# Kernel optimization log

Measured on AMD Instinct MI355X. Metric: run time of the kernel, lower is better.

## Reference

```python
import jax, jax.numpy as jnp
import numpy as np

DIM = 1024
HEADS = 16
HEAD_DIM = DIM // HEADS
B, N = 2, 2048


def setup_inputs() -> dict:
    key = jax.random.key(0)
    k1, k2, k3, k4 = jax.random.split(key, 4)
    scale = 1.0 / np.sqrt(DIM)
    return {
        "x": jax.random.normal(k1, (B, N, DIM), dtype=jnp.float32),
        "w_qkv": jax.random.normal(k2, (DIM, 3 * DIM), dtype=jnp.float32) * scale,
        "w_out": jax.random.normal(k3, (DIM, DIM), dtype=jnp.float32) * scale,
        "b_out": jax.random.normal(k4, (DIM,), dtype=jnp.float32) * 0.01,
    }


def reference(x, w_qkv, w_out, b_out):
    b, n, c = x.shape
    h, d = HEADS, c // HEADS
    sm_scale = d ** -0.5
    qkv = x @ w_qkv  # [b, n, 3c]
    q, k, v = jnp.split(qkv, 3, axis=-1)
    # [b, n, c] -> [b, h, n, d]
    q = q.reshape(b, n, h, d).transpose(0, 2, 1, 3)
    k = k.reshape(b, n, h, d).transpose(0, 2, 1, 3)
    v = v.reshape(b, n, h, d).transpose(0, 2, 1, 3)
    dots = jnp.einsum("bhqd,bhkd->bhqk", q, k) * sm_scale
    attn = jax.nn.softmax(dots, axis=-1)
    out = jnp.einsum("bhqk,bhkd->bhqd", attn, v)
    out = out.transpose(0, 2, 1, 3).reshape(b, n, c)
    return out @ w_out + b_out
```

## Files before the change

kernel.cpp:

```cpp
#include <hip/hip_runtime.h>
#include <hip/hip_bf16.h>

typedef __attribute__((ext_vector_type(8))) short bf16x8;
typedef __attribute__((ext_vector_type(4))) float f32x4;

#define B_    2
#define N_    2048
#define DIM_  1024
#define H_    16
#define D_    64
#define BH_   32
#define QSC   0.18033688f

static __device__ __forceinline__ void gload_lds16(const void* g, void* l) {
  __builtin_amdgcn_global_load_lds((const __attribute__((address_space(1))) void*)g,
                                   (__attribute__((address_space(3))) void*)l, 16, 0, 0);
}

__global__ __launch_bounds__(256) void prep_kernel(const float* __restrict__ x,
                                                   const float* __restrict__ w_qkv,
                                                   const float* __restrict__ w_out,
                                                   __hip_bfloat16* __restrict__ xb,
                                                   __hip_bfloat16* __restrict__ wqkT,
                                                   __hip_bfloat16* __restrict__ woT) {
  __shared__ float tile[64][65];
  const int bid = blockIdx.x, t = threadIdx.x;
  if (bid < 4096) {
    const int i = bid * 256 + t;
    float4 v = reinterpret_cast<const float4*>(x)[i];
    union { __hip_bfloat16 h[4]; uint2 u; } cv;
    cv.h[0] = __float2bfloat16(v.x);
    cv.h[1] = __float2bfloat16(v.y);
    cv.h[2] = __float2bfloat16(v.z);
    cv.h[3] = __float2bfloat16(v.w);
    reinterpret_cast<uint2*>(xb)[i] = cv.u;
    return;
  }
  const float* in;
  __hip_bfloat16* out;
  int R, C, c0, r0;
  if (bid < 4096 + 768) {
    const int bx = bid - 4096;
    in = w_qkv; out = wqkT; R = 1024; C = 3072;
    c0 = (bx % 48) * 64; r0 = (bx / 48) * 64;
  } else {
    const int bx = bid - 4096 - 768;
    in = w_out; out = woT; R = 1024; C = 1024;
    c0 = (bx % 16) * 64; r0 = (bx / 16) * 64;
  }
#pragma unroll
  for (int i = 0; i < 16; ++i) {
    int idx = i * 256 + t;
    int r = idx >> 6, c = idx & 63;
    tile[r][c] = in[(size_t)(r0 + r) * C + (c0 + c)];
  }
  __syncthreads();
#pragma unroll
  for (int i = 0; i < 16; ++i) {
    int idx = i * 256 + t;
    int rr = idx >> 6, cc = idx & 63;
    out[(size_t)(c0 + rr) * R + (r0 + cc)] = __float2bfloat16(tile[cc][rr]);
  }
}

#define GEMM_CORE(A_, Bt_)                                                               \
  constexpr int K = 1024;                                                                \
  __shared__ __align__(16) __hip_bfloat16 As[128 * 64];                                  \
  __shared__ __align__(16) __hip_bfloat16 Bs[128 * 64];                                  \
  const int t = threadIdx.x, w = t >> 6, lane = t & 63;                                  \
  const int l16 = lane & 15, kg = lane >> 4;                                             \
  const int m0 = blockIdx.y * 128, n0 = blockIdx.x * 128;                                \
  const int wm = w >> 1, wn = w & 1;                                                     \
  f32x4 acc[4][4];                                                                       \
  _Pragma("unroll") for (int i = 0; i < 4; ++i)                                          \
    _Pragma("unroll") for (int j = 0; j < 4; ++j) acc[i][j] = {0.f, 0.f, 0.f, 0.f};      \
  size_t srcA[4], srcB[4];                                                               \
  _Pragma("unroll") for (int i = 0; i < 4; ++i) {                                        \
    const int c = 256 * i + t;                                                           \
    const int row = c >> 3, jsw = (c & 7) ^ (row & 7);                                   \
    srcA[i] = (size_t)(m0 + row) * K + jsw * 8;                                          \
    srcB[i] = (size_t)(n0 + row) * K + jsw * 8;                                          \
  }                                                                                      \
  for (int k0 = 0; k0 < K; k0 += 64) {                                                   \
    __syncthreads();                                                                     \
    _Pragma("unroll") for (int i = 0; i < 4; ++i) {                                      \
      gload_lds16(A_ + srcA[i] + k0, (char*)As + 4096 * i + 1024 * w);                   \
      gload_lds16(Bt_ + srcB[i] + k0, (char*)Bs + 4096 * i + 1024 * w);                  \
    }                                                                                    \
    __syncthreads();                                                                     \
    _Pragma("unroll") for (int kk = 0; kk < 2; ++kk) {                                   \
      bf16x8 a[4], b[4];                                                                 \
      _Pragma("unroll") for (int i = 0; i < 4; ++i) {                                    \
        const int row = wm * 64 + i * 16 + l16;                                          \
        const int jsw = ((kk << 2) | kg) ^ (row & 7);                                    \
        a[i] = *reinterpret_cast<const bf16x8*>((const char*)As + row * 128 + jsw * 16); \
      }                                                                                  \
      _Pragma("unroll") for (int j = 0; j < 4; ++j) {                                    \
        const int row = wn * 64 + j * 16 + l16;                                          \
        const int jsw = ((kk << 2) | kg) ^ (row & 7);                                    \
        b[j] = *reinterpret_cast<const bf16x8*>((const char*)Bs + row * 128 + jsw * 16); \
      }                                                                                  \
      _Pragma("unroll") for (int i = 0; i < 4; ++i)                                      \
        _Pragma("unroll") for (int j = 0; j < 4; ++j)                                    \
          acc[i][j] = __builtin_amdgcn_mfma_f32_16x16x32_bf16(a[i], b[j], acc[i][j], 0, 0, 0); \
    }                                                                                    \
  }

__global__ __launch_bounds__(512, 2) void gemm_qkv_kernel(const __hip_bfloat16* __restrict__ A,
                                                          const __hip_bfloat16* __restrict__ Bt,
                                                          __hip_bfloat16* __restrict__ Qw,
                                                          __hip_bfloat16* __restrict__ Kw,
                                                          __hip_bfloat16* __restrict__ Vt) {
  __shared__ __align__(16) char lds[131072];
  const int t = threadIdx.x, w = t >> 6, lane = t & 63;
  const int l16 = lane & 15, kg = lane >> 4;
  int flat = blockIdx.y * 12 + blockIdx.x;
  flat = (flat & 7) * 24 + (flat >> 3);
  const int bx = flat % 12, by = flat / 12;
  const int m0 = by * 256, n0 = bx * 256;
  const int wm = w >> 2, wn = w & 3;
  const int rA = t >> 3;
  const int jb = (t & 7) ^ (rA & 7);

#define LDSOFF(bb, mat) (((bb) * 2 + (mat)) * 32768)
#define STG_A(bb, tt, h)                                                                    \
  do {                                                                                      \
    gload_lds16(A + (size_t)(m0 + rA + 64 * (h)) * 1024 + (tt) * 64 + jb * 8,               \
                (char*)lds + LDSOFF(bb, 0) + (h) * 8192 + t * 16);                          \
    gload_lds16(A + (size_t)(m0 + rA + 64 * (h) + 128) * 1024 + (tt) * 64 + jb * 8,         \
                (char*)lds + LDSOFF(bb, 0) + (h) * 8192 + 16384 + t * 16);                  \
  } while (0)
#define STG_B(bb, tt, h)                                                                    \
  do {                                                                                      \
    gload_lds16(Bt + (size_t)(n0 + rA + 128 * (h)) * 1024 + (tt) * 64 + jb * 8,             \
                (char*)lds + LDSOFF(bb, 1) + (h) * 16384 + t * 16);                         \
    gload_lds16(Bt + (size_t)(n0 + rA + 128 * (h) + 64) * 1024 + (tt) * 64 + jb * 8,        \
                (char*)lds + LDSOFF(bb, 1) + (h) * 16384 + 8192 + t * 16);                  \
  } while (0)
#define RD_A(dst, q, i, kk)                                                                 \
  {                                                                                         \
    const int row = wm * 128 + ((q) * 2 + (i)) * 16 + l16;                                  \
    dst = *reinterpret_cast<const bf16x8*>(Ab + row * 128 + ((((kk) * 4 + kg) ^ (row & 7)) * 16)); \
  }
#define RD_B(dst, nj, kk)                                                                   \
  {                                                                                         \
    const int row = wn * 64 + (nj) * 16 + l16;                                              \
    dst = *reinterpret_cast<const bf16x8*>(Bb + row * 128 + ((((kk) * 4 + kg) ^ (row & 7)) * 16)); \
  }
#define PHASE(q)                                                                            \
  do {                                                                                      \
    bf16x8 af[2][2];                                                                        \
    _Pragma("unroll") for (int i = 0; i < 2; ++i)                                           \
      _Pragma("unroll") for (int kk = 0; kk < 2; ++kk) RD_A(af[i][kk], q, i, kk);           \
    __builtin_amdgcn_s_setprio(1);                                                          \
    _Pragma("unroll") for (int i = 0; i < 2; ++i)                                           \
      _Pragma("unroll") for (int nj = 0; nj < 4; ++nj)                                      \
        _Pragma("unroll") for (int kk = 0; kk < 2; ++kk)                                    \
          acc[(q) * 2 + i][nj] =                                                            \
              __builtin_amdgcn_mfma_f32_16x16x32_bf16(af[i][kk], bfr[nj][kk],               \
                                                      acc[(q) * 2 + i][nj], 0, 0, 0);       \
    __builtin_amdgcn_s_setprio(0);                                                          \
  } while (0)

  f32x4 acc[8][4];
#pragma unroll
  for (int i = 0; i < 8; ++i)
#pragma unroll
    for (int j = 0; j < 4; ++j) acc[i][j] = {0.f, 0.f, 0.f, 0.f};

  STG_A(0, 0, 0); STG_A(0, 0, 1); STG_B(0, 0, 0); STG_B(0, 0, 1);
  STG_B(1, 1, 0); STG_B(1, 1, 1); STG_A(1, 1, 0);

#pragma unroll 1
  for (int kt = 0; kt < 16; ++kt) {
    const int b = kt & 1;
    const char* Ab = (const char*)lds + LDSOFF(b, 0);
    const char* Bb = (const char*)lds + LDSOFF(b, 1);

    if (kt < 15) STG_A(b ^ 1, kt + 1, 1);
    __builtin_amdgcn_sched_barrier(0);
    if (kt < 15) asm volatile("s_waitcnt vmcnt(8)" ::: "memory");
    else         asm volatile("s_waitcnt vmcnt(0)" ::: "memory");
    __builtin_amdgcn_s_barrier();
    __builtin_amdgcn_sched_barrier(0);
    bf16x8 bfr[4][2];
#pragma unroll
    for (int nj = 0; nj < 4; ++nj)
#pragma unroll
      for (int kk = 0; kk < 2; ++kk) RD_B(bfr[nj][kk], nj, kk);
    PHASE(0);
    __builtin_amdgcn_s_barrier();
    __builtin_amdgcn_sched_barrier(0);

    if (kt < 14) STG_B(b, kt + 2, 0);
    __builtin_amdgcn_sched_barrier(0);
    PHASE(1);
    __builtin_amdgcn_s_barrier();
    __builtin_amdgcn_sched_barrier(0);

    if (kt < 14) STG_B(b, kt + 2, 1);
    PHASE(2);

    if (kt < 14) STG_A(b, kt + 2, 0);
    __builtin_amdgcn_sched_barrier(0);
    PHASE(3);
    __builtin_amdgcn_s_barrier();
    __builtin_amdgcn_sched_barrier(0);
  }

  const int which = n0 >> 10;
#pragma unroll
  for (int nj = 0; nj < 4; ++nj) {
    const int n = n0 + wn * 64 + nj * 16 + l16;
    const int nn = n & 1023;
    const int h = nn >> 6, d = nn & 63;
#pragma unroll
    for (int mi = 0; mi < 8; ++mi) {
      const int m = m0 + wm * 128 + mi * 16 + kg * 4;
      const int bb = m >> 11, tt = m & 2047;
      if (which == 2) {
        union { __hip_bfloat16 hh[4]; unsigned long long u; } pv;
#pragma unroll
        for (int r = 0; r < 4; ++r) pv.hh[r] = __float2bfloat16(acc[mi][nj][r]);
        *reinterpret_cast<unsigned long long*>(
            &Vt[((size_t)(bb * H_ + h) * D_ + d) * N_ + tt]) = pv.u;
      } else {
        __hip_bfloat16* dst = (which == 0) ? Qw : Kw;
        const float sc = (which == 0) ? QSC : 1.0f;
#pragma unroll
        for (int r = 0; r < 4; ++r)
          dst[((size_t)(bb * H_ + h) * N_ + tt + r) * D_ + d] = __float2bfloat16(acc[mi][nj][r] * sc);
      }
    }
  }
#undef PHASE
#undef RD_B
#undef RD_A
#undef STG_B
#undef STG_A
#undef LDSOFF
}

__global__ __launch_bounds__(256) void gemm_out_kernel(const __hip_bfloat16* __restrict__ A,
                                                       const __hip_bfloat16* __restrict__ Bt,
                                                       const float* __restrict__ bo,
                                                       float* __restrict__ out) {
  GEMM_CORE(A, Bt)

#pragma unroll
  for (int j = 0; j < 4; ++j) {
    const int n = n0 + wn * 64 + j * 16 + l16;
    const float bias = bo[n];
#pragma unroll
    for (int i = 0; i < 4; ++i) {
#pragma unroll
      for (int r = 0; r < 4; ++r) {
        const int m = m0 + wm * 64 + i * 16 + kg * 4 + r;
        out[(size_t)m * 1024 + n] = acc[i][j][r] + bias;
      }
    }
  }
}

__global__ __launch_bounds__(512) void attn_kernel(const __hip_bfloat16* __restrict__ Q,
                                                   const __hip_bfloat16* __restrict__ K,
                                                   const __hip_bfloat16* __restrict__ Vt,
                                                   __hip_bfloat16* __restrict__ O) {
  __shared__ __align__(16) __hip_bfloat16 Ks[2][64 * 64];
  __shared__ __align__(16) __hip_bfloat16 Vs[2][64 * 64];
  __shared__ __align__(16) __hip_bfloat16 Plds[8][16][64];
  const int bh = blockIdx.y;
  const int q0 = blockIdx.x * 128;
  const int t = threadIdx.x, w = t >> 6, lane = t & 63;
  const int l16 = lane & 15, kg = lane >> 4;
  const int b = bh >> 4, h = bh & 15;

  const __hip_bfloat16* Kbh = K + (size_t)bh * N_ * D_;
  const __hip_bfloat16* Vbh = Vt + (size_t)bh * D_ * N_;

  const int crow = t >> 3, cb = t & 7;
  const int csw = cb ^ (crow & 7);
  const size_t offK = (size_t)crow * D_ + csw * 8;
  const size_t offV = (size_t)crow * N_ + csw * 8;

  const __hip_bfloat16* Qp = Q + ((size_t)bh * N_ + q0 + w * 16 + l16) * D_ + kg * 8;
  const bf16x8 qf0 = *reinterpret_cast<const bf16x8*>(Qp);
  const bf16x8 qf1 = *reinterpret_cast<const bf16x8*>(Qp + 32);

  bf16x8 ones;
#pragma unroll
  for (int i = 0; i < 8; ++i) ones[i] = (short)0x3F80;

  f32x4 oaccS = {0.f, 0.f, 0.f, 0.f};
  f32x4 oacc[4];
#pragma unroll
  for (int dn = 0; dn < 4; ++dn) oacc[dn] = {0.f, 0.f, 0.f, 0.f};

#define STAGE(bufi, kv)                                                          \
  do {                                                                           \
    gload_lds16(Kbh + (size_t)(kv) * D_ + offK, (char*)Ks[bufi] + w * 1024);     \
    gload_lds16(Vbh + (kv) + offV,              (char*)Vs[bufi] + w * 1024);     \
  } while (0)

  STAGE(0, 0);
  asm volatile("s_waitcnt vmcnt(0)" ::: "memory");
  __builtin_amdgcn_s_barrier();

#pragma unroll 1
  for (int it = 0; it < N_ / 64; ++it) {
    const int buf = it & 1;
    if (it + 1 < N_ / 64) STAGE(buf ^ 1, (it + 1) * 64);

    const char* Kb = (const char*)Ks[buf];
    const char* Vb = (const char*)Vs[buf];

    f32x4 s[4];
#pragma unroll
    for (int kt = 0; kt < 4; ++kt) s[kt] = {0.f, 0.f, 0.f, 0.f};
    __builtin_amdgcn_s_setprio(1);
#pragma unroll
    for (int kt = 0; kt < 4; ++kt) {
      const int row = kt * 16 + l16;
      const int rsw = (row & 7) << 4;
      const bf16x8 k0 = *reinterpret_cast<const bf16x8*>(Kb + row * 128 + ((kg << 4) ^ rsw));
      const bf16x8 k1 = *reinterpret_cast<const bf16x8*>(Kb + row * 128 + (((4 + kg) << 4) ^ rsw));
      s[kt] = __builtin_amdgcn_mfma_f32_16x16x32_bf16(k0, qf0, s[kt], 0, 0, 0);
      s[kt] = __builtin_amdgcn_mfma_f32_16x16x32_bf16(k1, qf1, s[kt], 0, 0, 0);
    }
    __builtin_amdgcn_s_setprio(0);

    const int xm3 = (l16 & 7) << 3;
#pragma unroll
    for (int kt = 0; kt < 4; ++kt) {
      union { __hip_bfloat16 hh[4]; unsigned long long u; } pk;
#pragma unroll
      for (int r = 0; r < 4; ++r) pk.hh[r] = __float2bfloat16(__builtin_amdgcn_exp2f(s[kt][r]));
      *reinterpret_cast<unsigned long long*>(&Plds[w][l16][(16 * kt + 4 * kg) ^ xm3]) = pk.u;
    }

    __builtin_amdgcn_s_setprio(1);
#pragma unroll
    for (int kk = 0; kk < 2; ++kk) {
      const bf16x8 pa = *reinterpret_cast<const bf16x8*>(
          &Plds[w][l16][(kk * 32 + kg * 8) ^ xm3]);
      oaccS = __builtin_amdgcn_mfma_f32_16x16x32_bf16(pa, ones, oaccS, 0, 0, 0);
#pragma unroll
      for (int dn = 0; dn < 4; ++dn) {
        const int vrow = dn * 16 + l16;
        const int vsw = (vrow & 7) << 4;
        const bf16x8 vf = *reinterpret_cast<const bf16x8*>(
            Vb + vrow * 128 + ((kk * 64 + kg * 16) ^ vsw));
        oacc[dn] = __builtin_amdgcn_mfma_f32_16x16x32_bf16(pa, vf, oacc[dn], 0, 0, 0);
      }
    }
    __builtin_amdgcn_s_setprio(0);

    asm volatile("s_waitcnt vmcnt(0)" ::: "memory");
    __builtin_amdgcn_s_barrier();
  }
#undef STAGE

  float inv[4];
#pragma unroll
  for (int r = 0; r < 4; ++r) inv[r] = 1.0f / oaccS[r];
  __hip_bfloat16* Ob = O + ((size_t)b * N_ + q0 + w * 16) * DIM_ + h * D_;
#pragma unroll
  for (int dn = 0; dn < 4; ++dn)
#pragma unroll
    for (int r = 0; r < 4; ++r)
      Ob[(size_t)(kg * 4 + r) * DIM_ + dn * 16 + l16] = __float2bfloat16(oacc[dn][r] * inv[r]);
}

extern "C" void kernel_launch(void* const* d_in, const int* in_sizes, int n_in,
                              void* d_out, int out_size, void* d_ws, size_t ws_size,
                              hipStream_t stream) {
  const float* x = (const float*)d_in[0];
  const float* w_qkv = (const float*)d_in[1];
  const float* w_out = (const float*)d_in[2];
  const float* b_out = (const float*)d_in[3];
  float* out = (float*)d_out;

  __hip_bfloat16* ws = (__hip_bfloat16*)d_ws;
  __hip_bfloat16* xb = ws;
  __hip_bfloat16* wqkT = xb + (size_t)4096 * 1024;
  __hip_bfloat16* woT = wqkT + (size_t)3072 * 1024;
  __hip_bfloat16* Qw = woT + (size_t)1024 * 1024;
  __hip_bfloat16* Kw = Qw + (size_t)BH_ * N_ * D_;
  __hip_bfloat16* Vt = Kw + (size_t)BH_ * N_ * D_;
  __hip_bfloat16* Ow = Vt + (size_t)BH_ * N_ * D_;

  prep_kernel<<<5120, 256, 0, stream>>>(x, w_qkv, w_out, xb, wqkT, woT);
  gemm_qkv_kernel<<<dim3(12, 16), 512, 0, stream>>>(xb, wqkT, Qw, Kw, Vt);
  attn_kernel<<<dim3(16, 32), 512, 0, stream>>>(Qw, Kw, Vt, Ow);
  gemm_out_kernel<<<dim3(8, 32), 256, 0, stream>>>(Ow, woT, b_out, out);
}
```

Baseline: 115.3 us.

## Double-buffer out-proj GEMM, triple-buffer attention KV, and compute softmax denominators with shuffles

Replaces the single-buffered out-projection GEMM macro with a double-buffered LDS pipeline. It issues the next K-tile load before waiting on the current one and raises MFMA priority. The attention kernel moves from two to three KV buffers with a prefetch distance of two and one barrier per iteration. The row-sum MFMA against a ones vector is replaced by fp32 sums of the exp values reduced with lane shuffles at the end. This gives more load/compute overlap and fewer MFMAs, at the cost of more LDS per block (which may lower occupancy) and a denominator computed in fp32 rather than from bf16-rounded probabilities.

```diff
diff --git a/kernel.cpp b/kernel.cpp
--- a/kernel.cpp
+++ b/kernel.cpp
@@ -62,49 +62,6 @@
     out[(size_t)(c0 + rr) * R + (r0 + cc)] = __float2bfloat16(tile[cc][rr]);
   }
 }
-
-#define GEMM_CORE(A_, Bt_)                                                               \
-  constexpr int K = 1024;                                                                \
-  __shared__ __align__(16) __hip_bfloat16 As[128 * 64];                                  \
-  __shared__ __align__(16) __hip_bfloat16 Bs[128 * 64];                                  \
-  const int t = threadIdx.x, w = t >> 6, lane = t & 63;                                  \
-  const int l16 = lane & 15, kg = lane >> 4;                                             \
-  const int m0 = blockIdx.y * 128, n0 = blockIdx.x * 128;                                \
-  const int wm = w >> 1, wn = w & 1;                                                     \
-  f32x4 acc[4][4];                                                                       \
-  _Pragma("unroll") for (int i = 0; i < 4; ++i)                                          \
-    _Pragma("unroll") for (int j = 0; j < 4; ++j) acc[i][j] = {0.f, 0.f, 0.f, 0.f};      \
-  size_t srcA[4], srcB[4];                                                               \
-  _Pragma("unroll") for (int i = 0; i < 4; ++i) {                                        \
-    const int c = 256 * i + t;                                                           \
-    const int row = c >> 3, jsw = (c & 7) ^ (row & 7);                                   \
-    srcA[i] = (size_t)(m0 + row) * K + jsw * 8;                                          \
-    srcB[i] = (size_t)(n0 + row) * K + jsw * 8;                                          \
-  }                                                                                      \
-  for (int k0 = 0; k0 < K; k0 += 64) {                                                   \
-    __syncthreads();                                                                     \
-    _Pragma("unroll") for (int i = 0; i < 4; ++i) {                                      \
-      gload_lds16(A_ + srcA[i] + k0, (char*)As + 4096 * i + 1024 * w);                   \
-      gload_lds16(Bt_ + srcB[i] + k0, (char*)Bs + 4096 * i + 1024 * w);                  \
-    }                                                                                    \
-    __syncthreads();                                                                     \
-    _Pragma("unroll") for (int kk = 0; kk < 2; ++kk) {                                   \
-      bf16x8 a[4], b[4];                                                                 \
-      _Pragma("unroll") for (int i = 0; i < 4; ++i) {                                    \
-        const int row = wm * 64 + i * 16 + l16;                                          \
-        const int jsw = ((kk << 2) | kg) ^ (row & 7);                                    \
-        a[i] = *reinterpret_cast<const bf16x8*>((const char*)As + row * 128 + jsw * 16); \
-      }                                                                                  \
-      _Pragma("unroll") for (int j = 0; j < 4; ++j) {                                    \
-        const int row = wn * 64 + j * 16 + l16;                                          \
-        const int jsw = ((kk << 2) | kg) ^ (row & 7);                                    \
-        b[j] = *reinterpret_cast<const bf16x8*>((const char*)Bs + row * 128 + jsw * 16); \
-      }                                                                                  \
-      _Pragma("unroll") for (int i = 0; i < 4; ++i)                                      \
-        _Pragma("unroll") for (int j = 0; j < 4; ++j)                                    \
-          acc[i][j] = __builtin_amdgcn_mfma_f32_16x16x32_bf16(a[i], b[j], acc[i][j], 0, 0, 0); \
-    }                                                                                    \
-  }
 
 __global__ __launch_bounds__(512, 2) void gemm_qkv_kernel(const __hip_bfloat16* __restrict__ A,
                                                           const __hip_bfloat16* __restrict__ Bt,
@@ -245,7 +202,74 @@
                                                        const __hip_bfloat16* __restrict__ Bt,
                                                        const float* __restrict__ bo,
                                                        float* __restrict__ out) {
-  GEMM_CORE(A, Bt)
+  __shared__ __align__(16) char lds[65536];
+  const int t = threadIdx.x, w = t >> 6, lane = t & 63;
+  const int l16 = lane & 15, kg = lane >> 4;
+  const int m0 = blockIdx.y * 128, n0 = blockIdx.x * 128;
+  const int wm = w >> 1, wn = w & 1;
+
+  f32x4 acc[4][4];
+#pragma unroll
+  for (int i = 0; i < 4; ++i)
+#pragma unroll
+    for (int j = 0; j < 4; ++j) acc[i][j] = {0.f, 0.f, 0.f, 0.f};
+
+  size_t srcA[4], srcB[4];
+#pragma unroll
+  for (int i = 0; i < 4; ++i) {
+    const int c = 256 * i + t;
+    const int row = c >> 3, jsw = (c & 7) ^ (row & 7);
+    srcA[i] = (size_t)(m0 + row) * 1024 + jsw * 8;
+    srcB[i] = (size_t)(n0 + row) * 1024 + jsw * 8;
+  }
+#define OSTG(bb, k0)                                                          \
+  do {                                                                        \
+    _Pragma("unroll") for (int i = 0; i < 4; ++i) {                           \
+      gload_lds16(A + srcA[i] + (k0), (char*)lds + (bb) * 32768 + i * 4096 + w * 1024);          \
+      gload_lds16(Bt + srcB[i] + (k0), (char*)lds + (bb) * 32768 + 16384 + i * 4096 + w * 1024); \
+    }                                                                         \
+  } while (0)
+
+  OSTG(0, 0);
+
+#pragma unroll 1
+  for (int kt = 0; kt < 16; ++kt) {
+    const int b = kt & 1;
+    __builtin_amdgcn_s_barrier();
+    __builtin_amdgcn_sched_barrier(0);
+    if (kt + 1 < 16) OSTG(b ^ 1, (kt + 1) * 64);
+    __builtin_amdgcn_sched_barrier(0);
+    if (kt + 1 < 16) asm volatile("s_waitcnt vmcnt(8)" ::: "memory");
+    else             asm volatile("s_waitcnt vmcnt(0)" ::: "memory");
+    __builtin_amdgcn_s_barrier();
+    __builtin_amdgcn_sched_barrier(0);
+    const char* Ab = (const char*)lds + b * 32768;
+    const char* Bb = (const char*)lds + b * 32768 + 16384;
+#pragma unroll
+    for (int kk = 0; kk < 2; ++kk) {
+      bf16x8 a[4], bfr[4];
+#pragma unroll
+      for (int i = 0; i < 4; ++i) {
+        const int row = wm * 64 + i * 16 + l16;
+        const int jsw = ((kk << 2) | kg) ^ (row & 7);
+        a[i] = *reinterpret_cast<const bf16x8*>(Ab + row * 128 + jsw * 16);
+      }
+#pragma unroll
+      for (int j = 0; j < 4; ++j) {
+        const int row = wn * 64 + j * 16 + l16;
+        const int jsw = ((kk << 2) | kg) ^ (row & 7);
+        bfr[j] = *reinterpret_cast<const bf16x8*>(Bb + row * 128 + jsw * 16);
+      }
+      __builtin_amdgcn_s_setprio(1);
+#pragma unroll
+      for (int i = 0; i < 4; ++i)
+#pragma unroll
+        for (int j = 0; j < 4; ++j)
+          acc[i][j] = __builtin_amdgcn_mfma_f32_16x16x32_bf16(a[i], bfr[j], acc[i][j], 0, 0, 0);
+      __builtin_amdgcn_s_setprio(0);
+    }
+  }
+#undef OSTG
 
 #pragma unroll
   for (int j = 0; j < 4; ++j) {
@@ -266,8 +290,8 @@
                                                    const __hip_bfloat16* __restrict__ K,
                                                    const __hip_bfloat16* __restrict__ Vt,
                                                    __hip_bfloat16* __restrict__ O) {
-  __shared__ __align__(16) __hip_bfloat16 Ks[2][64 * 64];
-  __shared__ __align__(16) __hip_bfloat16 Vs[2][64 * 64];
+  __shared__ __align__(16) __hip_bfloat16 Ks[3][64 * 64];
+  __shared__ __align__(16) __hip_bfloat16 Vs[3][64 * 64];
   __shared__ __align__(16) __hip_bfloat16 Plds[8][16][64];
   const int bh = blockIdx.y;
   const int q0 = blockIdx.x * 128;
@@ -287,11 +311,7 @@
   const bf16x8 qf0 = *reinterpret_cast<const bf16x8*>(Qp);
   const bf16x8 qf1 = *reinterpret_cast<const bf16x8*>(Qp + 32);
 
-  bf16x8 ones;
-#pragma unroll
-  for (int i = 0; i < 8; ++i) ones[i] = (short)0x3F80;
-
-  f32x4 oaccS = {0.f, 0.f, 0.f, 0.f};
+  float dacc = 0.f;
   f32x4 oacc[4];
 #pragma unroll
   for (int dn = 0; dn < 4; ++dn) oacc[dn] = {0.f, 0.f, 0.f, 0.f};
@@ -303,16 +323,19 @@
   } while (0)
 
   STAGE(0, 0);
-  asm volatile("s_waitcnt vmcnt(0)" ::: "memory");
-  __builtin_amdgcn_s_barrier();
+  STAGE(1, 64);
 
 #pragma unroll 1
   for (int it = 0; it < N_ / 64; ++it) {
-    const int buf = it & 1;
-    if (it + 1 < N_ / 64) STAGE(buf ^ 1, (it + 1) * 64);
-
-    const char* Kb = (const char*)Ks[buf];
-    const char* Vb = (const char*)Vs[buf];
+    if (it < N_ / 64 - 1) asm volatile("s_waitcnt vmcnt(2)" ::: "memory");
+    else                  asm volatile("s_waitcnt vmcnt(0)" ::: "memory");
+    __builtin_amdgcn_s_barrier();
+    __builtin_amdgcn_sched_barrier(0);
+    if (it + 2 < N_ / 64) STAGE((it + 2) % 3, (it + 2) * 64);
+    __builtin_amdgcn_sched_barrier(0);
+
+    const char* Kb = (const char*)Ks[it % 3];
+    const char* Vb = (const char*)Vs[it % 3];
 
     f32x4 s[4];
 #pragma unroll
@@ -330,20 +353,26 @@
     __builtin_amdgcn_s_setprio(0);
 
     const int xm3 = (l16 & 7) << 3;
+    float ds = 0.f;
 #pragma unroll
     for (int kt = 0; kt < 4; ++kt) {
-      union { __hip_bfloat16 hh[4]; unsigned long long u; } pk;
-#pragma unroll
-      for (int r = 0; r < 4; ++r) pk.hh[r] = __float2bfloat16(__builtin_amdgcn_exp2f(s[kt][r]));
+      const float p0 = __builtin_amdgcn_exp2f(s[kt][0]);
+      const float p1 = __builtin_amdgcn_exp2f(s[kt][1]);
+      const float p2 = __builtin_amdgcn_exp2f(s[kt][2]);
+      const float p3 = __builtin_amdgcn_exp2f(s[kt][3]);
+      ds += (p0 + p1) + (p2 + p3);
+      union { __hip_bfloat162 h2[2]; unsigned long long u; } pk;
+      pk.h2[0] = __float22bfloat162_rn(make_float2(p0, p1));
+      pk.h2[1] = __float22bfloat162_rn(make_float2(p2, p3));
       *reinterpret_cast<unsigned long long*>(&Plds[w][l16][(16 * kt + 4 * kg) ^ xm3]) = pk.u;
     }
+    dacc += ds;
 
     __builtin_amdgcn_s_setprio(1);
 #pragma unroll
     for (int kk = 0; kk < 2; ++kk) {
       const bf16x8 pa = *reinterpret_cast<const bf16x8*>(
           &Plds[w][l16][(kk * 32 + kg * 8) ^ xm3]);
-      oaccS = __builtin_amdgcn_mfma_f32_16x16x32_bf16(pa, ones, oaccS, 0, 0, 0);
 #pragma unroll
       for (int dn = 0; dn < 4; ++dn) {
         const int vrow = dn * 16 + l16;
@@ -354,15 +383,15 @@
       }
     }
     __builtin_amdgcn_s_setprio(0);
-
-    asm volatile("s_waitcnt vmcnt(0)" ::: "memory");
-    __builtin_amdgcn_s_barrier();
   }
 #undef STAGE
 
+  float dtot = dacc + __shfl_xor(dacc, 16);
+  dtot += __shfl_xor(dtot, 32);
   float inv[4];
 #pragma unroll
-  for (int r = 0; r < 4; ++r) inv[r] = 1.0f / oaccS[r];
+  for (int r = 0; r < 4; ++r) inv[r] = 1.0f / __shfl(dtot, kg * 4 + r);
+
   __hip_bfloat16* Ob = O + ((size_t)b * N_ + q0 + w * 16) * DIM_ + h * D_;
 #pragma unroll
   for (int dn = 0; dn < 4; ++dn)
```

Result: no change. 116.3 us (+0.8%).
